# Optimization experiments

Hardware: AMD Instinct MI355X
Metric: run time of the kernel (lower is better)

The kernel has to match this reference:

```python
import jax, jax.numpy as jnp
import numpy as np

GAMMA = 1.1
PC_MIN_XY, PC_MAX_XY = -75.2, 75.2


def setup_inputs() -> dict:
    key = jax.random.key(0)
    k1, k2, k3, k4, k5 = jax.random.split(key, 5)
    N, B, F = 200000, 256, 5
    # points: x,y in pc range, z in [-2,4], remaining features small
    xy = jax.random.uniform(k1, (N, 2), minval=PC_MIN_XY, maxval=PC_MAX_XY)
    z = jax.random.uniform(k2, (N, 1), minval=-2.0, maxval=4.0)
    feat = jax.random.normal(k3, (N, F - 3)) * 0.1
    cur_points = jnp.concatenate([xy, z, feat], axis=-1).astype(jnp.float32)
    # boxes: cx,cy,cz, dx,dy (sizes ~1..6 m), dz, heading
    centers = jax.random.uniform(k4, (B, 3), minval=PC_MIN_XY, maxval=PC_MAX_XY)
    sizes = jax.random.uniform(k5, (B, 3), minval=1.0, maxval=6.0)
    heading = jnp.zeros((B, 1), dtype=jnp.float32)
    cur_boxes = jnp.concatenate([centers, sizes, heading], axis=-1).astype(jnp.float32)
    return {"cur_points": cur_points, "cur_boxes": cur_boxes, "num_sample": 128}


def reference(cur_points, cur_boxes, num_sample):
    # cylindrical_pool: radius-mask + topk + gather (N >= num_sample, so no pad)
    # radii of cylinders: ||(dx,dy)/2|| * gamma  -> [B]
    cur_radiis = jnp.linalg.norm(cur_boxes[:, 3:5] * 0.5, axis=-1) * GAMMA
    # pairwise xy distance [B, N]
    dis = jnp.linalg.norm(cur_points[None, :, :2] - cur_boxes[:, None, :2], axis=-1)
    point_mask = (dis <= cur_radiis[:, None]).astype(cur_points.dtype)  # [B, N]
    # topk over 0/1 mask: in-radius points first (ties -> lowest index, like torch)
    sampled_mask, sampled_idx = jax.lax.top_k(point_mask, num_sample)  # [B, S]
    sampled_points = cur_points[sampled_idx]  # [B, S, F] gather
    sampled_points = jnp.where(sampled_mask[..., None] > 0, sampled_points, 0.0)
    return sampled_points
```

## Files before the change

### kernel.cpp

```cpp
#include <hip/hip_runtime.h>

#define GAMMA_F 1.1f
#define F_DIM 5
#define BOXG 8
#define MAX_NSEG 256
#define MAXL 1024

typedef float f32x2 __attribute__((ext_vector_type(2)));

__device__ __forceinline__ f32x2 pk_add(f32x2 a, f32x2 b) {
  f32x2 d;
  asm("v_pk_add_f32 %0, %1, %2" : "=v"(d) : "v"(a), "v"(b));
  return d;
}
__device__ __forceinline__ f32x2 pk_mul(f32x2 a, f32x2 b) {
  f32x2 d;
  asm("v_pk_mul_f32 %0, %1, %2" : "=v"(d) : "v"(a), "v"(b));
  return d;
}

__device__ __forceinline__ int prefix_lt(unsigned long long m) {
  return __builtin_amdgcn_mbcnt_hi(
      (unsigned)(m >> 32), __builtin_amdgcn_mbcnt_lo((unsigned)m, 0u));
}

template <int NWAVE>
__global__ void __launch_bounds__(NWAVE * 64, 4) seg_lds_kernel(
    const float* __restrict__ pts, const float* __restrict__ boxes,
    int* __restrict__ cnt, unsigned short* __restrict__ idx, int N, int S,
    int NSEG, int L, int NGRP) {
  __shared__ __align__(16) float rawf[MAXL * 5 + 4];
  __shared__ float sx[MAXL + 128];
  __shared__ float sy[MAXL + 128];

  const int tid = threadIdx.x;
  const int lane = tid & 63;
  const int wid = tid >> 6;
  const int bpg = NGRP / NWAVE;
  const int seg = blockIdx.x / bpg;
  const int bg = blockIdx.x - seg * bpg;
  const int grp = bg * NWAVE + wid;
  const int box0 = grp * BOXG;

  const int start = seg * L;
  const int end = min(start + L, N);
  const int npts = end - start;

  {
    const int dwStart = start * 5;
    const int dwEnd = dwStart + npts * 5;
    const int a0 = dwStart & ~3;
    const int totDw = dwEnd - a0;
    const int k4 = totDw >> 2;
    const float4* __restrict__ g4 = (const float4*)(pts + a0);
    float4* __restrict__ r4 = (float4*)rawf;
    for (int k = tid; k < k4; k += NWAVE * 64) r4[k] = g4[k];
    for (int d = a0 + (k4 << 2) + tid; d < dwEnd; d += NWAVE * 64)
      rawf[d - a0] = pts[d];
    __syncthreads();
    const int off0 = dwStart - a0;
    for (int t = tid; t < npts; t += NWAVE * 64) {
      sx[t] = rawf[off0 + t * 5];
      sy[t] = rawf[off0 + t * 5 + 1];
    }
  }

  f32x2 ncx2[BOXG], ncy2[BOXG];
  float smax[BOXG];
#pragma unroll
  for (int b = 0; b < BOXG; ++b) {
    const float* bx = boxes + (box0 + b) * 7;
    const float cx = bx[0];
    const float cy = bx[1];
    ncx2[b][0] = -cx;
    ncx2[b][1] = -cx;
    ncy2[b][0] = -cy;
    ncy2[b][1] = -cy;
    const float hdx = __fmul_rn(bx[3], 0.5f);
    const float hdy = __fmul_rn(bx[4], 0.5f);
    const float r = __fmul_rn(
        __fsqrt_rn(__fadd_rn(__fmul_rn(hdx, hdx), __fmul_rn(hdy, hdy))),
        GAMMA_F);
    const unsigned ru = __float_as_uint(r);
    const float rsucc = __uint_as_float(ru + 1u);
    const double m = ((double)r + (double)rsucc) * 0.5;
    const double m2 = m * m;
    const bool incl = ((ru & 1u) == 0u);
    const float c1 = (float)m2;
    const double c1d = (double)c1;
    const bool keep = incl ? (c1d <= m2) : (c1d < m2);
    smax[b] = keep ? c1 : __uint_as_float(__float_as_uint(c1) - 1u);
  }
  __syncthreads();

  int c[BOXG];
#pragma unroll
  for (int b = 0; b < BOXG; ++b) c[b] = 0;

  const size_t ibase = ((size_t)box0 * NSEG + seg) * S;
  const int nfull = npts / 128;

#define PROCESS_8(RELBASE, XX, YY, G0, G1)                          \
  {                                                                 \
    const int rel = (RELBASE) + 2 * lane;                           \
    _Pragma("unroll") for (int b = 0; b < BOXG; ++b) {              \
      const f32x2 dxx = pk_add((XX), ncx2[b]);                      \
      const f32x2 dyy = pk_add((YY), ncy2[b]);                      \
      const f32x2 mxx = pk_mul(dxx, dxx);                           \
      const f32x2 myy = pk_mul(dyy, dyy);                           \
      const f32x2 ss = pk_add(mxx, myy);                            \
      const bool sel0 = (G0) && (ss[0] <= smax[b]);                 \
      const bool sel1 = (G1) && (ss[1] <= smax[b]);                 \
      const unsigned long long m0 = __ballot(sel0);                 \
      const unsigned long long m1 = __ballot(sel1);                 \
      if (m0 | m1) {                                                \
        const int p0 = prefix_lt(m0);                               \
        const int p1 = prefix_lt(m1);                               \
        const int r0 = c[b] + p0 + p1;                              \
        const int r1 = c[b] + p0 + (sel0 ? 1 : 0) + p1;             \
        unsigned short* mp = idx + ibase + (size_t)b * NSEG * S;    \
        if (sel0 && r0 < S) mp[r0] = (unsigned short)rel;           \
        if (sel1 && r1 < S) mp[r1] = (unsigned short)(rel + 1);     \
        c[b] += __popcll(m0) + __popcll(m1);                        \
      }                                                             \
    }                                                               \
  }

  for (int it = 0; it < nfull; ++it) {
    const f32x2 xx = *(const f32x2*)&sx[it * 128 + 2 * lane];
    const f32x2 yy = *(const f32x2*)&sy[it * 128 + 2 * lane];
    PROCESS_8(it * 128, xx, yy, true, true);
  }
  const int relb = nfull * 128;
  if (relb < npts) {
    const f32x2 xx = *(const f32x2*)&sx[relb + 2 * lane];
    const f32x2 yy = *(const f32x2*)&sy[relb + 2 * lane];
    const int rel = relb + 2 * lane;
    const bool g0 = (rel < npts);
    const bool g1 = (rel + 1 < npts);
    PROCESS_8(relb, xx, yy, g0, g1);
  }
#undef PROCESS_8

  if (lane == 0) {
#pragma unroll
    for (int b = 0; b < BOXG; ++b) cnt[(box0 + b) * NSEG + seg] = min(c[b], S);
  }
}

__global__ void __launch_bounds__(256) gather_kernel(
    const float* __restrict__ pts, const int* __restrict__ cnt,
    const unsigned short* __restrict__ idx, float* __restrict__ out, int N,
    int S, int NSEG, int L) {
  const int b = blockIdx.x;
  const int tid = threadIdx.x;
  const int lane = tid & 63;
  const int wid = tid >> 6;

  __shared__ int pfx[MAX_NSEG + 1];
  __shared__ int wtot[4];
  __shared__ int woff[4];

  int v = (tid < NSEG) ? cnt[b * NSEG + tid] : 0;
  int sv = v;
#pragma unroll
  for (int d = 1; d < 64; d <<= 1) {
    const int t = __shfl_up(sv, d, 64);
    if (lane >= d) sv += t;
  }
  if (lane == 63) wtot[wid] = sv;
  __syncthreads();
  if (tid == 0) {
    int a = 0;
#pragma unroll
    for (int w = 0; w < 4; ++w) {
      woff[w] = a;
      a += wtot[w];
    }
  }
  __syncthreads();
  const int incl = sv + woff[wid];
  if (tid < NSEG) pfx[tid + 1] = incl;
  if (tid == 0) pfx[0] = 0;
  __syncthreads();

  const int total = pfx[NSEG];
  if (tid < S) {
    float* o = out + ((size_t)b * S + tid) * F_DIM;
    if (tid < total) {
      int lo = 0, hi = NSEG - 1;
      while (lo < hi) {
        const int mid = (lo + hi + 1) >> 1;
        if (pfx[mid] <= tid) lo = mid;
        else hi = mid - 1;
      }
      const int s = lo;
      const int gi =
          s * L + (int)idx[((size_t)b * NSEG + s) * S + (tid - pfx[s])];
      const float* p = pts + (size_t)gi * F_DIM;
      o[0] = p[0];
      o[1] = p[1];
      o[2] = p[2];
      o[3] = p[3];
      o[4] = p[4];
    } else {
      o[0] = 0.0f;
      o[1] = 0.0f;
      o[2] = 0.0f;
      o[3] = 0.0f;
      o[4] = 0.0f;
    }
  }
}

template <int BLOCK>
__global__ void __launch_bounds__(BLOCK) voxel_sampler_fallback(
    const float* __restrict__ pts, const float* __restrict__ boxes,
    float* __restrict__ out, int N, int S) {
  constexpr int NW = BLOCK / 64;
  const int b = blockIdx.x;
  const int tid = threadIdx.x;
  const int lane = tid & 63;
  const int wid = tid >> 6;

  const float cx = boxes[b * 7 + 0];
  const float cy = boxes[b * 7 + 1];
  const float hdx = __fmul_rn(boxes[b * 7 + 3], 0.5f);
  const float hdy = __fmul_rn(boxes[b * 7 + 4], 0.5f);
  const float r = __fmul_rn(
      __fsqrt_rn(__fadd_rn(__fmul_rn(hdx, hdx), __fmul_rn(hdy, hdy))),
      GAMMA_F);

  __shared__ int s_wsum[NW];
  __shared__ int s_count;
  if (tid == 0) s_count = 0;
  __syncthreads();

  float* outb = out + (size_t)b * S * F_DIM;

  for (int base = 0; base < N; base += BLOCK) {
    const int i = base + tid;
    bool sel = false;
    float x = 0.0f, y = 0.0f;
    if (i < N) {
      x = pts[i * F_DIM + 0];
      y = pts[i * F_DIM + 1];
      const float ddx = __fsub_rn(x, cx);
      const float ddy = __fsub_rn(y, cy);
      const float dis =
          __fsqrt_rn(__fadd_rn(__fmul_rn(ddx, ddx), __fmul_rn(ddy, ddy)));
      sel = (dis <= r);
    }
    const unsigned long long m = __ballot(sel);
    if (lane == 0) s_wsum[wid] = __popcll(m);
    __syncthreads();
    const int cbase = s_count;
    int wbase = 0;
    int tot = 0;
#pragma unroll
    for (int w = 0; w < NW; ++w) {
      const int v = s_wsum[w];
      if (w < wid) wbase += v;
      tot += v;
    }
    const int pos = cbase + wbase + __popcll(m & ((1ULL << lane) - 1ULL));
    if (sel && pos < S) {
      float* o = outb + pos * F_DIM;
      o[0] = x;
      o[1] = y;
      o[2] = pts[i * F_DIM + 2];
      o[3] = pts[i * F_DIM + 3];
      o[4] = pts[i * F_DIM + 4];
    }
    __syncthreads();
    if (tid == 0) s_count = cbase + tot;
    __syncthreads();
    if (cbase + tot >= S) break;
  }

  __syncthreads();
  int cnt = s_count;
  if (cnt > S) cnt = S;
  for (int j = cnt * F_DIM + tid; j < S * F_DIM; j += BLOCK) outb[j] = 0.0f;
}

extern "C" void kernel_launch(void* const* d_in, const int* in_sizes, int n_in,
                              void* d_out, int out_size, void* d_ws,
                              size_t ws_size, hipStream_t stream) {
  const float* pts = (const float*)d_in[0];
  const float* boxes = (const float*)d_in[1];
  float* out = (float*)d_out;

  const int N = in_sizes[0] / F_DIM;
  const int B = in_sizes[1] / 7;
  const int S = out_size / (B * F_DIM);

  const int NSEG = 256;
  int L = ((N + NSEG - 1) / NSEG + 1) & ~1;
  const int NGRP = B / BOXG;
  constexpr int NWAVE = 16;

  const size_t sz_cnt = (size_t)B * NSEG * sizeof(int);
  const size_t off_idx = (sz_cnt + 255) & ~(size_t)255;
  const size_t sz_idx = (size_t)B * NSEG * S * sizeof(unsigned short);
  const size_t need = off_idx + sz_idx;

  const bool fast = (ws_size >= need) && (L >= 2) && (L <= MAXL) &&
                    (L - 1 <= 65535) && (B % BOXG == 0) && (S <= 256) &&
                    (NSEG <= MAX_NSEG) && (NGRP % NWAVE == 0) &&
                    ((size_t)L * NSEG >= (size_t)N);

  if (fast) {
    char* ws = (char*)d_ws;
    int* cnt = (int*)ws;
    unsigned short* idx = (unsigned short*)(ws + off_idx);

    const int bpg = NGRP / NWAVE;
    seg_lds_kernel<NWAVE><<<NSEG * bpg, NWAVE * 64, 0, stream>>>(
        pts, boxes, cnt, idx, N, S, NSEG, L, NGRP);
    gather_kernel<<<B, 256, 0, stream>>>(pts, cnt, idx, out, N, S, NSEG, L);
  } else {
    voxel_sampler_fallback<1024><<<B, 1024, 0, stream>>>(pts, boxes, out, N,
                                                         S);
  }
}
```

Baseline: 27.04 us.

## Stage point xy pairs directly into compact float4 LDS buffer

```diff
diff --git a/kernel.cpp b/kernel.cpp
--- a/kernel.cpp
+++ b/kernel.cpp
@@ -25,13 +25,11 @@
 }
 
 template <int NWAVE>
-__global__ void __launch_bounds__(NWAVE * 64, 4) seg_lds_kernel(
+__global__ void __launch_bounds__(NWAVE * 64, 8) seg_lds_kernel(
     const float* __restrict__ pts, const float* __restrict__ boxes,
     int* __restrict__ cnt, unsigned short* __restrict__ idx, int N, int S,
     int NSEG, int L, int NGRP) {
-  __shared__ __align__(16) float rawf[MAXL * 5 + 4];
-  __shared__ float sx[MAXL + 128];
-  __shared__ float sy[MAXL + 128];
+  __shared__ __align__(16) float4 sp[MAXL / 2 + 64];
 
   const int tid = threadIdx.x;
   const int lane = tid & 63;
@@ -45,25 +43,7 @@
   const int start = seg * L;
   const int end = min(start + L, N);
   const int npts = end - start;
-
-  {
-    const int dwStart = start * 5;
-    const int dwEnd = dwStart + npts * 5;
-    const int a0 = dwStart & ~3;
-    const int totDw = dwEnd - a0;
-    const int k4 = totDw >> 2;
-    const float4* __restrict__ g4 = (const float4*)(pts + a0);
-    float4* __restrict__ r4 = (float4*)rawf;
-    for (int k = tid; k < k4; k += NWAVE * 64) r4[k] = g4[k];
-    for (int d = a0 + (k4 << 2) + tid; d < dwEnd; d += NWAVE * 64)
-      rawf[d - a0] = pts[d];
-    __syncthreads();
-    const int off0 = dwStart - a0;
-    for (int t = tid; t < npts; t += NWAVE * 64) {
-      sx[t] = rawf[off0 + t * 5];
-      sy[t] = rawf[off0 + t * 5 + 1];
-    }
-  }
+  const int npair = npts >> 1;
 
   f32x2 ncx2[BOXG], ncy2[BOXG];
   float smax[BOXG];
@@ -90,6 +70,11 @@
     const double c1d = (double)c1;
     const bool keep = incl ? (c1d <= m2) : (c1d < m2);
     smax[b] = keep ? c1 : __uint_as_float(__float_as_uint(c1) - 1u);
+  }
+
+  for (int t = tid; t < npair; t += NWAVE * 64) {
+    const float* p0 = pts + (size_t)(start + 2 * t) * F_DIM;
+    sp[t] = make_float4(p0[0], p0[F_DIM], p0[1], p0[F_DIM + 1]);
   }
   __syncthreads();
 
@@ -127,14 +112,16 @@
   }
 
   for (int it = 0; it < nfull; ++it) {
-    const f32x2 xx = *(const f32x2*)&sx[it * 128 + 2 * lane];
-    const f32x2 yy = *(const f32x2*)&sy[it * 128 + 2 * lane];
+    const float4 q = sp[it * 64 + lane];
+    const f32x2 xx = {q.x, q.y};
+    const f32x2 yy = {q.z, q.w};
     PROCESS_8(it * 128, xx, yy, true, true);
   }
   const int relb = nfull * 128;
   if (relb < npts) {
-    const f32x2 xx = *(const f32x2*)&sx[relb + 2 * lane];
-    const f32x2 yy = *(const f32x2*)&sy[relb + 2 * lane];
+    const float4 q = sp[nfull * 64 + lane];
+    const f32x2 xx = {q.x, q.y};
+    const f32x2 yy = {q.z, q.w};
     const int rel = relb + 2 * lane;
     const bool g0 = (rel < npts);
     const bool g1 = (rel + 1 < npts);
@@ -308,7 +295,7 @@
   const bool fast = (ws_size >= need) && (L >= 2) && (L <= MAXL) &&
                     (L - 1 <= 65535) && (B % BOXG == 0) && (S <= 256) &&
                     (NSEG <= MAX_NSEG) && (NGRP % NWAVE == 0) &&
-                    ((size_t)L * NSEG >= (size_t)N);
+                    (N % 2 == 0) && ((size_t)L * NSEG >= (size_t)N);
 
   if (fast) {
     char* ws = (char*)d_ws;
```

Result: slower. 28.10 us (+3.9%).
